# Performance work log

Measured on AMD Instinct MI355X. Metric: run time of the kernel, lower is better.

The kernel has to match this reference:

```python
import jax, jax.numpy as jnp
import numpy as np

N = 100000
FEAT = 256
HID = 128
OUT = 64
E = 1600000


def setup_inputs() -> dict:
    key = jax.random.key(0)
    ks = jax.random.split(key, 8)
    x = jax.random.normal(ks[0], (N, FEAT), dtype=jnp.float32)
    edge_index = jax.random.randint(ks[1], (2, E), 0, N, dtype=jnp.int64)
    # Glorot-like weights, zero bias (PyG GCNConv default init style)
    def glorot(k, fin, fout):
        s = (6.0 / (fin + fout)) ** 0.5
        return jax.random.uniform(k, (fin, fout), jnp.float32, -s, s)
    return {
        "x": x,
        "edge_index": edge_index,
        "W1": glorot(ks[2], FEAT, HID), "b1": jnp.zeros((HID,), jnp.float32),
        "W2": glorot(ks[3], HID, HID), "b2": jnp.zeros((HID,), jnp.float32),
        "W3": glorot(ks[4], HID, OUT), "b3": jnp.zeros((OUT,), jnp.float32),
    }


def _gcn_prep(edge_index, n_nodes):
    # Add self-loops and compute symmetric normalization deg^-1/2 (PyG gcn_norm).
    loops = jnp.arange(n_nodes, dtype=edge_index.dtype)
    src = jnp.concatenate([edge_index[0], loops])
    dst = jnp.concatenate([edge_index[1], loops])
    ones = jnp.ones(src.shape[0], dtype=jnp.float32)
    deg = jax.ops.segment_sum(ones, dst, num_segments=n_nodes)
    dinv = jnp.where(deg > 0, jax.lax.rsqrt(jnp.maximum(deg, 1.0)), 0.0)
    norm = dinv[src] * dinv[dst]  # [E+N]
    return src, dst, norm


def _gcn_layer(x, src, dst, norm, W, b, n_nodes):
    h = x @ W                              # [N, F_out]
    msg = h[src] * norm[:, None]           # gather + edge scale
    out = jax.ops.segment_sum(msg, dst, num_segments=n_nodes)  # scatter-add
    return out + b


def reference(x, edge_index, W1, b1, W2, b2, W3, b3):
    n = x.shape[0]
    src, dst, norm = _gcn_prep(edge_index, n)
    h = jax.nn.relu(_gcn_layer(x, src, dst, norm, W1, b1, n))
    h = jax.nn.relu(_gcn_layer(h, src, dst, norm, W2, b2, n))
    return _gcn_layer(h, src, dst, norm, W3, b3, n)
```

## Files before the change

kernel.cpp:

```cpp
#include <hip/hip_runtime.h>
#include <hip/hip_bf16.h>


#define NNODES 100000
#define NB 391
#define PB 2048
#define BCAP 12288

typedef _Float16 half8  __attribute__((ext_vector_type(8)));
typedef _Float16 half4v __attribute__((ext_vector_type(4)));
typedef _Float16 half2v __attribute__((ext_vector_type(2)));
typedef float    floatx4 __attribute__((ext_vector_type(4)));

static __device__ __forceinline__ floatx4 h2f4(half4v v) {
    return (floatx4){(float)v.x, (float)v.y, (float)v.z, (float)v.w};
}

__global__ __launch_bounds__(256) void blockhist_k(const int* __restrict__ dst,
                                                   int* __restrict__ H, int e) {
    __shared__ int h[NB];
    for (int q = threadIdx.x; q < NB; q += 256) h[q] = 0;
    __syncthreads();
    int base = blockIdx.x * PB;
    int lim = e - base; if (lim > PB) lim = PB;
    for (int i = threadIdx.x; i < lim; i += 256)
        atomicAdd(&h[dst[base + i] >> 8], 1);
    __syncthreads();
    for (int q = threadIdx.x; q < NB; q += 256)
        H[(size_t)blockIdx.x * NB + q] = h[q];
}

__global__ __launch_bounds__(256) void bucketscan_k(const int* __restrict__ H,
                                                    int* __restrict__ O,
                                                    int* __restrict__ T, int npb) {
    __shared__ int lds[256];
    int b = blockIdx.x, t = threadIdx.x;
    int running = 0;
    for (int c0 = 0; c0 < npb; c0 += 256) {
        int idx = c0 + t;
        int v = (idx < npb) ? H[(size_t)idx * NB + b] : 0;
        lds[t] = v;
        __syncthreads();
        #pragma unroll
        for (int off = 1; off < 256; off <<= 1) {
            int u = (t >= off) ? lds[t - off] : 0;
            __syncthreads();
            lds[t] += u;
            __syncthreads();
        }
        int excl = lds[t] - v + running;
        if (idx < npb) O[(size_t)idx * NB + b] = excl;
        running += lds[255];
        __syncthreads();
    }
    if (t == 0) T[b] = running;
}

__global__ __launch_bounds__(512) void scanT_k(const int* __restrict__ T,
                                               int* __restrict__ bbase, int e) {
    __shared__ int lds[512];
    int t = threadIdx.x;
    int v = (t < NB) ? T[t] : 0;
    lds[t] = v;
    __syncthreads();
    #pragma unroll
    for (int off = 1; off < 512; off <<= 1) {
        int u = (t >= off) ? lds[t - off] : 0;
        __syncthreads();
        lds[t] += u;
        __syncthreads();
    }
    if (t < NB) bbase[t] = lds[t] - v;
    if (t == 0) bbase[NB] = e;
}

__global__ __launch_bounds__(256) void scatter_k(const int* __restrict__ src,
                                                 const int* __restrict__ dst,
                                                 const int* __restrict__ O,
                                                 const int* __restrict__ bbase,
                                                 unsigned* __restrict__ binned, int e) {
    __shared__ int cur[NB];
    for (int q = threadIdx.x; q < NB; q += 256)
        cur[q] = bbase[q] + O[(size_t)blockIdx.x * NB + q];
    __syncthreads();
    int base = blockIdx.x * PB;
    int lim = e - base; if (lim > PB) lim = PB;
    for (int i = threadIdx.x; i < lim; i += 256) {
        int d = dst[base + i];
        int s = src[base + i];
        int p = atomicAdd(&cur[d >> 8], 1);
        binned[p] = ((unsigned)(d & 255) << 17) | (unsigned)s;
    }
}

__global__ __launch_bounds__(256) void bucket_fill_k(
    const unsigned* __restrict__ binned, const int* __restrict__ bbase,
    int* __restrict__ rowptr, int* __restrict__ eidx,
    float* __restrict__ dinv, int n, int e) {
    __shared__ int cnt[256];
    __shared__ int cur[256];
    __shared__ int lds[256];
    __shared__ int sbuf[BCAP];
    int b = blockIdx.x, t = threadIdx.x;
    int beg = bbase[b], end = bbase[b + 1];
    int m = end - beg;
    cnt[t] = 0;
    __syncthreads();
    for (int q = t; q < m; q += 256) {
        unsigned r = binned[beg + q];
        atomicAdd(&cnt[r >> 17], 1);
    }
    __syncthreads();
    int v = cnt[t];
    lds[t] = v;
    __syncthreads();
    #pragma unroll
    for (int off = 1; off < 256; off <<= 1) {
        int u = (t >= off) ? lds[t - off] : 0;
        __syncthreads();
        lds[t] += u;
        __syncthreads();
    }
    int excl = lds[t] - v;
    int node = b * 256 + t;
    if (node < n) {
        rowptr[node] = beg + excl;
        dinv[node] = rsqrtf(1.0f + (float)v);
    }
    if (b == NB - 1 && t == 0) rowptr[n] = e;
    cur[t] = excl;
    __syncthreads();
    for (int q = t; q < m; q += 256) {
        unsigned r = binned[beg + q];
        int p = atomicAdd(&cur[r >> 17], 1);
        if (p < BCAP) sbuf[p] = (int)(r & 0x1FFFFu);
    }
    __syncthreads();
    for (int q = t; q < m; q += 256) eidx[beg + q] = sbuf[q];
}

__global__ __launch_bounds__(256) void castWt_k(
    const float* __restrict__ W1, const float* __restrict__ W2,
    const float* __restrict__ W3, _Float16* __restrict__ Wt1,
    _Float16* __restrict__ Wt2, _Float16* __restrict__ Wt3) {
    int i = blockIdx.x * 256 + threadIdx.x;
    if (i < 128 * 256) {
        int nn = i >> 8, k = i & 255;
        Wt1[i] = (_Float16)W1[k * 128 + nn];
    }
    if (i < 128 * 128) {
        int nn = i >> 7, k = i & 127;
        Wt2[i] = (_Float16)W2[k * 128 + nn];
    }
    if (i < 64 * 128) {
        int nn = i >> 7, k = i & 127;
        Wt3[i] = (_Float16)W3[k * 64 + nn];
    }
}

template<typename TA, int FIN, int FOUT>
__global__ __launch_bounds__(256, 2) void gemm_wave_k(
    const TA* __restrict__ X, const _Float16* __restrict__ Wt,
    const float* __restrict__ dinv, _Float16* __restrict__ G, int n)
{
    constexpr int NKC = FIN / 32;
    constexpr int NCT = FOUT / 64;
    const int wave = threadIdx.x >> 6;
    const int lane = threadIdx.x & 63;
    const int mrow = lane & 15;
    const int kq   = (lane >> 4) * 8;
    const int m0   = blockIdx.x * 16;

    int r = m0 + mrow; if (r > n - 1) r = n - 1;

    half8 af[NKC];
    if constexpr (sizeof(TA) == 4) {
        const float* xp = (const float*)X + (size_t)r * FIN + kq;
        float4 t[2 * NKC];
        #pragma unroll
        for (int kc = 0; kc < NKC; ++kc) {
            t[2 * kc]     = *(const float4*)(xp + kc * 32);
            t[2 * kc + 1] = *(const float4*)(xp + kc * 32 + 4);
        }
        #pragma unroll
        for (int kc = 0; kc < NKC; ++kc) {
            float4 u0 = t[2 * kc], u1 = t[2 * kc + 1];
            af[kc] = (half8){(_Float16)u0.x, (_Float16)u0.y, (_Float16)u0.z, (_Float16)u0.w,
                             (_Float16)u1.x, (_Float16)u1.y, (_Float16)u1.z, (_Float16)u1.w};
        }
    } else {
        const _Float16* xp = (const _Float16*)X + (size_t)r * FIN + kq;
        #pragma unroll
        for (int kc = 0; kc < NKC; ++kc)
            af[kc] = *(const half8*)(xp + kc * 32);
    }

    half8 bf[NCT][NKC];
    #pragma unroll
    for (int ct = 0; ct < NCT; ++ct) {
        const _Float16* wp = Wt + (size_t)((wave * NCT + ct) * 16 + mrow) * FIN + kq;
        #pragma unroll
        for (int kc = 0; kc < NKC; ++kc)
            bf[ct][kc] = *(const half8*)(wp + kc * 32);
    }

    floatx4 acc[NCT];
    #pragma unroll
    for (int ct = 0; ct < NCT; ++ct) acc[ct] = (floatx4){0.f, 0.f, 0.f, 0.f};
    #pragma unroll
    for (int kc = 0; kc < NKC; ++kc)
        #pragma unroll
        for (int ct = 0; ct < NCT; ++ct)
            acc[ct] = __builtin_amdgcn_mfma_f32_16x16x32_f16(af[kc], bf[ct][kc], acc[ct], 0, 0, 0);

    #pragma unroll
    for (int reg = 0; reg < 4; ++reg) {
        int rr = m0 + (lane >> 4) * 4 + reg;
        if (rr < n) {
            float s = dinv[rr];
            #pragma unroll
            for (int ct = 0; ct < NCT; ++ct)
                G[(size_t)rr * FOUT + (wave * NCT + ct) * 16 + mrow] =
                    (_Float16)(acc[ct][reg] * s);
        }
    }
}

template<bool RELU, typename OutT>
__global__ __launch_bounds__(256) void gather128_k(
    const _Float16* __restrict__ g, const int* __restrict__ rowptr,
    const int* __restrict__ eidx, const float* __restrict__ dinv,
    const float* __restrict__ bias, OutT* __restrict__ out, int n)
{
    int wave = threadIdx.x >> 6;
    int lane = threadIdx.x & 63;
    int half = lane >> 5;
    int hl   = lane & 31;
    int node = blockIdx.x * 4 + wave;
    if (node >= n) return;

    int beg = rowptr[node];
    int end = rowptr[node + 1];

    const half4v* g4 = (const half4v*)g;
    floatx4 aA = {0.f,0.f,0.f,0.f}, aB = aA, aC = aA, aD = aA;
    if (half == 0) aA = h2f4(g4[(size_t)node * 32 + hl]);

    for (int j0 = beg; j0 < end; j0 += 64) {
        int m = end - j0; if (m > 64) m = 64;
        int id = (lane < m) ? eidx[j0 + lane] : 0;
        int t = 0;
        for (; t + 7 < m; t += 8) {
            int i0 = __shfl(id, t + half);
            int i1 = __shfl(id, t + 2 + half);
            int i2 = __shfl(id, t + 4 + half);
            int i3 = __shfl(id, t + 6 + half);
            half4v v0 = g4[(size_t)i0 * 32 + hl];
            half4v v1 = g4[(size_t)i1 * 32 + hl];
            half4v v2 = g4[(size_t)i2 * 32 + hl];
            half4v v3 = g4[(size_t)i3 * 32 + hl];
            aA += h2f4(v0); aB += h2f4(v1); aC += h2f4(v2); aD += h2f4(v3);
        }
        for (; t + 1 < m; t += 2) {
            int i0 = __shfl(id, t + half);
            aA += h2f4(g4[(size_t)i0 * 32 + hl]);
        }
        if (t < m) {
            int i0 = __shfl(id, t);
            if (half == 0) aA += h2f4(g4[(size_t)i0 * 32 + hl]);
        }
    }
    aA += aB; aC += aD; aA += aC;
    aA.x += __shfl_down(aA.x, 32);
    aA.y += __shfl_down(aA.y, 32);
    aA.z += __shfl_down(aA.z, 32);
    aA.w += __shfl_down(aA.w, 32);

    if (half == 0) {
        float sc = dinv[node];
        float4 bb = *(const float4*)(bias + 4 * hl);
        float o0 = fmaf(aA.x, sc, bb.x);
        float o1 = fmaf(aA.y, sc, bb.y);
        float o2 = fmaf(aA.z, sc, bb.z);
        float o3 = fmaf(aA.w, sc, bb.w);
        if (RELU) {
            o0 = fmaxf(o0, 0.f); o1 = fmaxf(o1, 0.f);
            o2 = fmaxf(o2, 0.f); o3 = fmaxf(o3, 0.f);
        }
        if constexpr (sizeof(OutT) == 2) {
            ((half4v*)out)[(size_t)node * 32 + hl] =
                (half4v){(_Float16)o0, (_Float16)o1, (_Float16)o2, (_Float16)o3};
        } else {
            *(float4*)((float*)out + (size_t)node * 128 + 4 * hl) =
                make_float4(o0, o1, o2, o3);
        }
    }
}

template<bool RELU>
__global__ __launch_bounds__(256) void gather64_k(
    const _Float16* __restrict__ g, const int* __restrict__ rowptr,
    const int* __restrict__ eidx, const float* __restrict__ dinv,
    const float* __restrict__ bias, float* __restrict__ out, int n)
{
    int wave = threadIdx.x >> 6;
    int lane = threadIdx.x & 63;
    int half = lane >> 5;
    int hl   = lane & 31;
    int node = blockIdx.x * 4 + wave;
    if (node >= n) return;

    int beg = rowptr[node];
    int end = rowptr[node + 1];

    const half2v* g2 = (const half2v*)g;
    float ax=0.f, ay=0.f, bx=0.f, by=0.f, cx=0.f, cy=0.f, dx=0.f, dy=0.f;
    if (half == 0) {
        half2v v = g2[(size_t)node * 32 + hl];
        ax = (float)v.x; ay = (float)v.y;
    }

    for (int j0 = beg; j0 < end; j0 += 64) {
        int m = end - j0; if (m > 64) m = 64;
        int id = (lane < m) ? eidx[j0 + lane] : 0;
        int t = 0;
        for (; t + 7 < m; t += 8) {
            int i0 = __shfl(id, t + half);
            int i1 = __shfl(id, t + 2 + half);
            int i2 = __shfl(id, t + 4 + half);
            int i3 = __shfl(id, t + 6 + half);
            half2v v0 = g2[(size_t)i0 * 32 + hl];
            half2v v1 = g2[(size_t)i1 * 32 + hl];
            half2v v2 = g2[(size_t)i2 * 32 + hl];
            half2v v3 = g2[(size_t)i3 * 32 + hl];
            ax += (float)v0.x; ay += (float)v0.y;
            bx += (float)v1.x; by += (float)v1.y;
            cx += (float)v2.x; cy += (float)v2.y;
            dx += (float)v3.x; dy += (float)v3.y;
        }
        for (; t + 1 < m; t += 2) {
            int i0 = __shfl(id, t + half);
            half2v v0 = g2[(size_t)i0 * 32 + hl];
            ax += (float)v0.x; ay += (float)v0.y;
        }
        if (t < m) {
            int i0 = __shfl(id, t);
            if (half == 0) {
                half2v v0 = g2[(size_t)i0 * 32 + hl];
                ax += (float)v0.x; ay += (float)v0.y;
            }
        }
    }
    ax += bx + cx + dx; ay += by + cy + dy;
    ax += __shfl_down(ax, 32);
    ay += __shfl_down(ay, 32);

    if (half == 0) {
        float sc = dinv[node];
        float2 bb = *(const float2*)(bias + 2 * hl);
        float ox = fmaf(ax, sc, bb.x);
        float oy = fmaf(ay, sc, bb.y);
        if (RELU) { ox = fmaxf(ox, 0.f); oy = fmaxf(oy, 0.f); }
        *(float2*)(out + (size_t)node * 64 + 2 * hl) = make_float2(ox, oy);
    }
}

extern "C" void kernel_launch(void* const* d_in, const int* in_sizes, int n_in,
                              void* d_out, int out_size, void* d_ws, size_t ws_size,
                              hipStream_t stream) {
    const float* x  = (const float*)d_in[0];
    const int*   ei = (const int*)d_in[1];
    const float* W1 = (const float*)d_in[2];
    const float* b1 = (const float*)d_in[3];
    const float* W2 = (const float*)d_in[4];
    const float* b2 = (const float*)d_in[5];
    const float* W3 = (const float*)d_in[6];
    const float* b3 = (const float*)d_in[7];
    float* out = (float*)d_out;

    const int N = NNODES;
    const int E = in_sizes[1] / 2;
    const int* srcI = ei;
    const int* dstI = ei + E;

    const int npb = (E + PB - 1) / PB;

    char* ws = (char*)d_ws;
    size_t p = 0;
    auto alloc = [&](size_t bytes) { void* r = ws + p; p = (p + bytes + 255) & ~(size_t)255; return r; };
    float*     dinv   = (float*)    alloc((size_t)N * 4);
    int*       rowptr = (int*)      alloc((size_t)(N + 1) * 4);
    int*       bbase  = (int*)      alloc((size_t)(NB + 1) * 4);
    int*       T      = (int*)      alloc((size_t)NB * 4);
    int*       H      = (int*)      alloc((size_t)npb * NB * 4);
    int*       O      = (int*)      alloc((size_t)npb * NB * 4);
    unsigned*  binned = (unsigned*) alloc((size_t)E * 4);
    int*       eidx   = (int*)      alloc((size_t)E * 4);
    _Float16*  Wt1    = (_Float16*) alloc((size_t)128 * 256 * 2);
    _Float16*  Wt2    = (_Float16*) alloc((size_t)128 * 128 * 2);
    _Float16*  Wt3    = (_Float16*) alloc((size_t)64 * 128 * 2);
    _Float16*  A      = (_Float16*) alloc((size_t)N * 128 * 2);
    _Float16*  Ch     = (_Float16*) alloc((size_t)N * 128 * 2);

    const int nb_node4 = (N + 3) / 4;
    const int nb_gemm = (N + 15) / 16;

    blockhist_k<<<npb, 256, 0, stream>>>(dstI, H, E);
    castWt_k<<<128, 256, 0, stream>>>(W1, W2, W3, Wt1, Wt2, Wt3);
    bucketscan_k<<<NB, 256, 0, stream>>>(H, O, T, npb);
    scanT_k<<<1, 512, 0, stream>>>(T, bbase, E);
    scatter_k<<<npb, 256, 0, stream>>>(srcI, dstI, O, bbase, binned, E);
    bucket_fill_k<<<NB, 256, 0, stream>>>(binned, bbase, rowptr, eidx, dinv, N, E);

    gemm_wave_k<float, 256, 128><<<nb_gemm, 256, 0, stream>>>(x, Wt1, dinv, A, N);
    gather128_k<true, _Float16><<<nb_node4, 256, 0, stream>>>(A, rowptr, eidx, dinv, b1, Ch, N);

    gemm_wave_k<_Float16, 128, 128><<<nb_gemm, 256, 0, stream>>>(Ch, Wt2, dinv, A, N);
    gather128_k<true, _Float16><<<nb_node4, 256, 0, stream>>>(A, rowptr, eidx, dinv, b2, Ch, N);

    gemm_wave_k<_Float16, 128, 64><<<nb_gemm, 256, 0, stream>>>(Ch, Wt3, dinv, A, N);
    gather64_k<false><<<nb_node4, 256, 0, stream>>>(A, rowptr, eidx, dinv, b3, out, N);
}
```

Before: 525.3 us.

## Stage pre-swizzled fp16 weights in LDS and give each wave its own rows

Weights are now cast into an MFMA-fragment order so each lane reads one contiguous half8 per tile. Each GEMM block copies the whole weight matrix into LDS once and computes 64 rows, with every wave covering all output columns for 16 rows. Before, each wave held a quarter of the columns of a 16-row tile and reloaded its weight slice from global memory. This cuts repeated weight fetches and quarters the number of blocks, at the cost of up to 64KB LDS per block, which may limit occupancy for the first layer, plus a block-wide barrier.

```diff
diff --git a/kernel.cpp b/kernel.cpp
--- a/kernel.cpp
+++ b/kernel.cpp
@@ -139,52 +139,65 @@
     for (int q = t; q < m; q += 256) eidx[beg + q] = sbuf[q];
 }
 
-__global__ __launch_bounds__(256) void castWt_k(
+static __device__ __forceinline__ void cast_frag(
+    const float* __restrict__ W, _Float16* __restrict__ Wf,
+    int FIN, int FOUT, int i) {
+    int k = i / FOUT, n = i % FOUT;
+    int ct = n >> 4, mrow = n & 15;
+    int kc = k >> 5, hi = (k & 31) >> 3, j = k & 7;
+    int NKC = FIN / 32;
+    int idx = ((ct * NKC + kc) * 64 + hi * 16 + mrow) * 8 + j;
+    Wf[idx] = (_Float16)W[(size_t)k * FOUT + n];
+}
+
+__global__ __launch_bounds__(256) void castW_k(
     const float* __restrict__ W1, const float* __restrict__ W2,
-    const float* __restrict__ W3, _Float16* __restrict__ Wt1,
-    _Float16* __restrict__ Wt2, _Float16* __restrict__ Wt3) {
+    const float* __restrict__ W3, _Float16* __restrict__ Wf1,
+    _Float16* __restrict__ Wf2, _Float16* __restrict__ Wf3) {
     int i = blockIdx.x * 256 + threadIdx.x;
-    if (i < 128 * 256) {
-        int nn = i >> 8, k = i & 255;
-        Wt1[i] = (_Float16)W1[k * 128 + nn];
-    }
-    if (i < 128 * 128) {
-        int nn = i >> 7, k = i & 127;
-        Wt2[i] = (_Float16)W2[k * 128 + nn];
-    }
-    if (i < 64 * 128) {
-        int nn = i >> 7, k = i & 127;
-        Wt3[i] = (_Float16)W3[k * 64 + nn];
-    }
+    if (i < 256 * 128) cast_frag(W1, Wf1, 256, 128, i);
+    if (i < 128 * 128) cast_frag(W2, Wf2, 128, 128, i);
+    if (i < 128 * 64)  cast_frag(W3, Wf3, 128, 64, i);
 }
 
 template<typename TA, int FIN, int FOUT>
-__global__ __launch_bounds__(256, 2) void gemm_wave_k(
-    const TA* __restrict__ X, const _Float16* __restrict__ Wt,
+__global__ __launch_bounds__(256, 2) void gemm_ldsB_k(
+    const TA* __restrict__ X, const _Float16* __restrict__ Wf,
     const float* __restrict__ dinv, _Float16* __restrict__ G, int n)
 {
     constexpr int NKC = FIN / 32;
-    constexpr int NCT = FOUT / 64;
-    const int wave = threadIdx.x >> 6;
-    const int lane = threadIdx.x & 63;
+    constexpr int NCT = FOUT / 16;
+    __shared__ _Float16 wS[FOUT * FIN];
+
+    const int tid  = threadIdx.x;
+    const int wave = tid >> 6;
+    const int lane = tid & 63;
     const int mrow = lane & 15;
     const int kq   = (lane >> 4) * 8;
-    const int m0   = blockIdx.x * 16;
-
-    int r = m0 + mrow; if (r > n - 1) r = n - 1;
+
+    {
+        const half8* s = (const half8*)Wf;
+        half8* d = (half8*)wS;
+        constexpr int TOT8 = FOUT * FIN / 8;
+        #pragma unroll
+        for (int i = tid; i < TOT8; i += 256) d[i] = s[i];
+    }
+
+    int r = blockIdx.x * 64 + wave * 16 + mrow;
+    if (r > n - 1) r = n - 1;
 
     half8 af[NKC];
     if constexpr (sizeof(TA) == 4) {
         const float* xp = (const float*)X + (size_t)r * FIN + kq;
-        float4 t[2 * NKC];
+        float4 t0[NKC], t1[NKC];
         #pragma unroll
         for (int kc = 0; kc < NKC; ++kc) {
-            t[2 * kc]     = *(const float4*)(xp + kc * 32);
-            t[2 * kc + 1] = *(const float4*)(xp + kc * 32 + 4);
+            t0[kc] = *(const float4*)(xp + kc * 32);
+            t1[kc] = *(const float4*)(xp + kc * 32 + 4);
         }
         #pragma unroll
         for (int kc = 0; kc < NKC; ++kc) {
-            float4 u0 = t[2 * kc], u1 = t[2 * kc + 1];
+            float4 u0 = t0[kc], u1 = t1[kc];
             af[kc] = (half8){(_Float16)u0.x, (_Float16)u0.y, (_Float16)u0.z, (_Float16)u0.w,
                              (_Float16)u1.x, (_Float16)u1.y, (_Float16)u1.z, (_Float16)u1.w};
         }
@@ -195,33 +208,30 @@
             af[kc] = *(const half8*)(xp + kc * 32);
     }
 
-    half8 bf[NCT][NKC];
-    #pragma unroll
-    for (int ct = 0; ct < NCT; ++ct) {
-        const _Float16* wp = Wt + (size_t)((wave * NCT + ct) * 16 + mrow) * FIN + kq;
-        #pragma unroll
-        for (int kc = 0; kc < NKC; ++kc)
-            bf[ct][kc] = *(const half8*)(wp + kc * 32);
-    }
+    __syncthreads();
 
     floatx4 acc[NCT];
     #pragma unroll
     for (int ct = 0; ct < NCT; ++ct) acc[ct] = (floatx4){0.f, 0.f, 0.f, 0.f};
+
     #pragma unroll
-    for (int kc = 0; kc < NKC; ++kc)
-        #pragma unroll
-        for (int ct = 0; ct < NCT; ++ct)
-            acc[ct] = __builtin_amdgcn_mfma_f32_16x16x32_f16(af[kc], bf[ct][kc], acc[ct], 0, 0, 0);
-
+    for (int kc = 0; kc < NKC; ++kc) {
+        #pragma unroll
+        for (int ct = 0; ct < NCT; ++ct) {
+            half8 bf = *(const half8*)&wS[(((ct * NKC) + kc) * 64 + lane) * 8];
+            acc[ct] = __builtin_amdgcn_mfma_f32_16x16x32_f16(af[kc], bf, acc[ct], 0, 0, 0);
+        }
+    }
+
+    int rbase = blockIdx.x * 64 + wave * 16 + (lane >> 4) * 4;
     #pragma unroll
     for (int reg = 0; reg < 4; ++reg) {
-        int rr = m0 + (lane >> 4) * 4 + reg;
+        int rr = rbase + reg;
         if (rr < n) {
             float s = dinv[rr];
             #pragma unroll
             for (int ct = 0; ct < NCT; ++ct)
-                G[(size_t)rr * FOUT + (wave * NCT + ct) * 16 + mrow] =
-                    (_Float16)(acc[ct][reg] * s);
+                G[(size_t)rr * FOUT + ct * 16 + mrow] = (_Float16)(acc[ct][reg] * s);
         }
     }
 }
@@ -396,28 +406,28 @@
     int*       O      = (int*)      alloc((size_t)npb * NB * 4);
     unsigned*  binned = (unsigned*) alloc((size_t)E * 4);
     int*       eidx   = (int*)      alloc((size_t)E * 4);
-    _Float16*  Wt1    = (_Float16*) alloc((size_t)128 * 256 * 2);
-    _Float16*  Wt2    = (_Float16*) alloc((size_t)128 * 128 * 2);
-    _Float16*  Wt3    = (_Float16*) alloc((size_t)64 * 128 * 2);
+    _Float16*  Wf1    = (_Float16*) alloc((size_t)128 * 256 * 2);
+    _Float16*  Wf2    = (_Float16*) alloc((size_t)128 * 128 * 2);
+    _Float16*  Wf3    = (_Float16*) alloc((size_t)64 * 128 * 2);
     _Float16*  A      = (_Float16*) alloc((size_t)N * 128 * 2);
     _Float16*  Ch     = (_Float16*) alloc((size_t)N * 128 * 2);
 
     const int nb_node4 = (N + 3) / 4;
-    const int nb_gemm = (N + 15) / 16;
+    const int nb_gemm = (N + 63) / 64;
 
     blockhist_k<<<npb, 256, 0, stream>>>(dstI, H, E);
-    castWt_k<<<128, 256, 0, stream>>>(W1, W2, W3, Wt1, Wt2, Wt3);
+    castW_k<<<128, 256, 0, stream>>>(W1, W2, W3, Wf1, Wf2, Wf3);
     bucketscan_k<<<NB, 256, 0, stream>>>(H, O, T, npb);
     scanT_k<<<1, 512, 0, stream>>>(T, bbase, E);
     scatter_k<<<npb, 256, 0, stream>>>(srcI, dstI, O, bbase, binned, E);
     bucket_fill_k<<<NB, 256, 0, stream>>>(binned, bbase, rowptr, eidx, dinv, N, E);
 
-    gemm_wave_k<float, 256, 128><<<nb_gemm, 256, 0, stream>>>(x, Wt1, dinv, A, N);
+    gemm_ldsB_k<float, 256, 128><<<nb_gemm, 256, 0, stream>>>(x, Wf1, dinv, A, N);
     gather128_k<true, _Float16><<<nb_node4, 256, 0, stream>>>(A, rowptr, eidx, dinv, b1, Ch, N);
 
-    gemm_wave_k<_Float16, 128, 128><<<nb_gemm, 256, 0, stream>>>(Ch, Wt2, dinv, A, N);
+    gemm_ldsB_k<_Float16, 128, 128><<<nb_gemm, 256, 0, stream>>>(Ch, Wf2, dinv, A, N);
     gather128_k<true, _Float16><<<nb_node4, 256, 0, stream>>>(A, rowptr, eidx, dinv, b2, Ch, N);
 
-    gemm_wave_k<_Float16, 128, 64><<<nb_gemm, 256, 0, stream>>>(Ch, Wt3, dinv, A, N);
+    gemm_ldsB_k<_Float16, 128, 64><<<nb_gemm, 256, 0, stream>>>(Ch, Wf3, dinv, A, N);
     gather64_k<false><<<nb_node4, 256, 0, stream>>>(A, rowptr, eidx, dinv, b3, out, N);
 }
```

After: 444.3 us. 15.4% less time.
